# Optimization experiments

Hardware: AMD Instinct MI355X
Metric: run time of the kernel (lower is better)

Reference implementation:

```python
import jax, jax.numpy as jnp
import numpy as np

VOCAB_SIZE = 64
HIDDEN_DIM = 64
SEQ_LEN = 48
MEMORY_SLOTS = 8
DECAY_THRESHOLD = 0.05
B = 131072


def setup_inputs() -> dict:
    key = jax.random.key(0)
    ks = jax.random.split(key, 8)
    seqs = jax.random.randint(ks[0], (B, SEQ_LEN), 0, VOCAB_SIZE, dtype=jnp.int64 if jax.config.jax_enable_x64 else jnp.int32)
    query_tok = jax.random.randint(ks[1], (B,), 0, VOCAB_SIZE, dtype=seqs.dtype)
    embed = jax.random.normal(ks[2], (VOCAB_SIZE + 2, HIDDEN_DIM), dtype=jnp.float32) * 0.02
    W1 = jax.random.normal(ks[3], (HIDDEN_DIM, HIDDEN_DIM * 2), dtype=jnp.float32) * (1.0 / np.sqrt(2 * HIDDEN_DIM))
    b1 = jnp.zeros((HIDDEN_DIM,), dtype=jnp.float32)
    W2 = jax.random.normal(ks[4], (VOCAB_SIZE, HIDDEN_DIM), dtype=jnp.float32) * (1.0 / np.sqrt(HIDDEN_DIM))
    b2 = jnp.zeros((VOCAB_SIZE,), dtype=jnp.float32)
    log_stability = jnp.asarray(np.log(10.0), dtype=jnp.float32)
    return {"seqs": seqs, "query_tok": query_tok, "embed": embed,
            "W1": W1, "b1": b1, "W2": W2, "b2": b2, "log_stability": log_stability}


def reference(seqs, query_tok, embed, W1, b1, W2, b2, log_stability):
    S = jnp.exp(log_stability)
    # Final memory after the per-step decay/evict loop: last MEMORY_SLOTS tokens
    # inserted at steps t0 = SEQ_LEN-1-MEMORY_SLOTS .. SEQ_LEN-2, with final
    # ages a = [MEMORY_SLOTS-1 .. 0]. Each entry has been scaled by
    # prod_{j=0..a} exp(-j/S) = exp(-a(a+1)/(2S)); retained iff exp(-a/S) >= thr.
    ages = jnp.arange(MEMORY_SLOTS - 1, -1, -1, dtype=jnp.float32)          # [M]
    toks = seqs[:, SEQ_LEN - 1 - MEMORY_SLOTS:SEQ_LEN - 1]                  # [B, M]
    embs = embed[toks]                                                      # [B, M, D]
    keep = (jnp.exp(-ages / S) >= DECAY_THRESHOLD)                          # [M] bool
    w = jnp.exp(-ages * (ages + 1.0) / (2.0 * S)) * keep.astype(jnp.float32)
    count = jnp.maximum(jnp.sum(keep.astype(jnp.float32)), 1.0)
    mem_summary = jnp.einsum('bmd,m->bd', embs, w) / count                  # [B, D]
    q_emb = embed[query_tok]                                                # [B, D]
    h = jnp.concatenate([q_emb, mem_summary], axis=-1)                      # [B, 2D]
    h = jax.nn.relu(h @ W1.T + b1)                                          # [B, D]
    logits = h @ W2.T + b2                                                  # [B, V]
    return logits
```

## Files before the change

### kernel.cpp

```cpp
#include <hip/hip_runtime.h>

#define VOCAB 64
#define HID 64
#define SEQL 48
#define MSLOTS 8
#define BLKT 256
#define STR 68

__global__ void ebb_prep(const float* __restrict__ embed,
                         const float* __restrict__ W1,
                         const float* __restrict__ b1,
                         const float* __restrict__ log_stab,
                         float* __restrict__ ws) {
    int t = blockIdx.x;
    int tid = threadIdx.x;
    int table = tid >> 6;
    int col = tid & 63;
    const float* erow = embed + t * HID;
    const float* wrow = W1 + col * (2 * HID) + table * HID;
    float acc = (table == 0) ? b1[col] : 0.f;
#pragma unroll
    for (int k = 0; k < HID; ++k) acc = fmaf(erow[k], wrow[k], acc);
    ws[table * (VOCAB * HID) + t * HID + col] = acc;

    if (blockIdx.x == 0 && tid < MSLOTS) {
        float S = expf(log_stab[0]);
        float cnt = 0.f;
        for (int m = 0; m < MSLOTS; ++m) {
            float age = (float)(MSLOTS - 1 - m);
            cnt += (expf(-age / S) >= 0.05f) ? 1.f : 0.f;
        }
        cnt = fmaxf(cnt, 1.f);
        float age = (float)(MSLOTS - 1 - tid);
        float keep = (expf(-age / S) >= 0.05f) ? 1.f : 0.f;
        float w = expf(-age * (age + 1.f) / (2.f * S)) * keep;
        ws[2 * VOCAB * HID + tid] = w / cnt;
    }
}

__global__ __launch_bounds__(BLKT, 2)
void ebb_main(const int* __restrict__ seqs, const int* __restrict__ qtok,
              const float* __restrict__ ws, const float* __restrict__ W2,
              const float* __restrict__ b2,
              float* __restrict__ out) {
    __shared__ float sWq[VOCAB][STR];
    __shared__ float sWm[VOCAB][STR];
    __shared__ float sH[64][STR];

    int tid  = threadIdx.x;
    int lane = tid & 63;
    int wv   = tid >> 6;

    for (int i = tid; i < VOCAB * HID; i += BLKT) {
        int r = i >> 6, c = i & 63;
        sWq[r][c] = ws[i];
        sWm[r][c] = ws[VOCAB * HID + i];
    }

    float4 w2r[16];
    {
        const float4* W2v = (const float4*)(W2 + lane * HID);
#pragma unroll
        for (int j4 = 0; j4 < 16; ++j4) w2r[j4] = W2v[j4];
    }
    float bb = b2[lane];

    int row = blockIdx.x * BLKT + tid;
    const int* srow = seqs + (size_t)row * SEQL;
    int qt = qtok[row];
    int t0 = srow[39];
    int4 ta = *(const int4*)(srow + 40);
    int4 tb = *(const int4*)(srow + 44);
    int toks[MSLOTS] = {t0, ta.x, ta.y, ta.z, ta.w, tb.x, tb.y, tb.z};

    __syncthreads();

    float h[HID];
    {
        const float4* wq = (const float4*)&sWq[qt][0];
#pragma unroll
        for (int j4 = 0; j4 < 16; ++j4) {
            float4 a = wq[j4];
            h[4 * j4 + 0] = a.x; h[4 * j4 + 1] = a.y;
            h[4 * j4 + 2] = a.z; h[4 * j4 + 3] = a.w;
        }
    }
#pragma unroll
    for (int m = 0; m < MSLOTS; ++m) {
        float wwm = ws[2 * VOCAB * HID + m];
        const float4* wm = (const float4*)&sWm[toks[m]][0];
#pragma unroll
        for (int j4 = 0; j4 < 16; ++j4) {
            float4 a = wm[j4];
            h[4 * j4 + 0] = fmaf(wwm, a.x, h[4 * j4 + 0]);
            h[4 * j4 + 1] = fmaf(wwm, a.y, h[4 * j4 + 1]);
            h[4 * j4 + 2] = fmaf(wwm, a.z, h[4 * j4 + 2]);
            h[4 * j4 + 3] = fmaf(wwm, a.w, h[4 * j4 + 3]);
        }
    }
#pragma unroll
    for (int j = 0; j < HID; ++j) h[j] = fmaxf(h[j], 0.f);

    size_t obase = (size_t)blockIdx.x * BLKT * HID;
#pragma unroll 1
    for (int c = 0; c < 4; ++c) {
        if (wv == c) {
            float4* dst = (float4*)&sH[lane][0];
#pragma unroll
            for (int j4 = 0; j4 < 16; ++j4)
                dst[j4] = make_float4(h[4 * j4 + 0], h[4 * j4 + 1],
                                      h[4 * j4 + 2], h[4 * j4 + 3]);
        }
        __syncthreads();
#pragma unroll 1
        for (int r = 0; r < 16; ++r) {
            int hr = wv * 16 + r;
            const float4* hv = (const float4*)&sH[hr][0];
            float a0 = bb, a1 = 0.f, a2 = 0.f, a3 = 0.f;
#pragma unroll
            for (int j4 = 0; j4 < 16; j4 += 4) {
                float4 x0 = hv[j4 + 0], x1 = hv[j4 + 1];
                float4 x2 = hv[j4 + 2], x3 = hv[j4 + 3];
                a0 = fmaf(x0.x, w2r[j4 + 0].x, a0); a0 = fmaf(x0.y, w2r[j4 + 0].y, a0);
                a0 = fmaf(x0.z, w2r[j4 + 0].z, a0); a0 = fmaf(x0.w, w2r[j4 + 0].w, a0);
                a1 = fmaf(x1.x, w2r[j4 + 1].x, a1); a1 = fmaf(x1.y, w2r[j4 + 1].y, a1);
                a1 = fmaf(x1.z, w2r[j4 + 1].z, a1); a1 = fmaf(x1.w, w2r[j4 + 1].w, a1);
                a2 = fmaf(x2.x, w2r[j4 + 2].x, a2); a2 = fmaf(x2.y, w2r[j4 + 2].y, a2);
                a2 = fmaf(x2.z, w2r[j4 + 2].z, a2); a2 = fmaf(x2.w, w2r[j4 + 2].w, a2);
                a3 = fmaf(x3.x, w2r[j4 + 3].x, a3); a3 = fmaf(x3.y, w2r[j4 + 3].y, a3);
                a3 = fmaf(x3.z, w2r[j4 + 3].z, a3); a3 = fmaf(x3.w, w2r[j4 + 3].w, a3);
            }
            out[obase + (size_t)(c * 64 + hr) * HID + lane] = (a0 + a1) + (a2 + a3);
        }
        __syncthreads();
    }
}

extern "C" void kernel_launch(void* const* d_in, const int* in_sizes, int n_in,
                              void* d_out, int out_size, void* d_ws, size_t ws_size,
                              hipStream_t stream) {
    const int*   seqs     = (const int*)d_in[0];
    const int*   qtok     = (const int*)d_in[1];
    const float* embed    = (const float*)d_in[2];
    const float* W1       = (const float*)d_in[3];
    const float* b1       = (const float*)d_in[4];
    const float* W2       = (const float*)d_in[5];
    const float* b2       = (const float*)d_in[6];
    const float* log_stab = (const float*)d_in[7];
    float* out = (float*)d_out;
    float* ws  = (float*)d_ws;

    int B = in_sizes[1];

    ebb_prep<<<VOCAB, 2 * HID, 0, stream>>>(embed, W1, b1, log_stab, ws);

    int nblk = (B + BLKT - 1) / BLKT;
    ebb_main<<<nblk, BLKT, 0, stream>>>(seqs, qtok, ws, W2, b2, out);
}
```

Baseline: 126.8 us.

## Stage all hidden rows in reused swizzled LDS and drop per-chunk barriers

Overlays the hidden-activation staging buffer on the same shared memory as the W1 lookup tables, using a 64KB buffer and an XOR swizzle to avoid bank conflicts. All 256 rows are written at once, so the four-round write/sync/compute loop becomes a single pass where each wave handles its own 64 rows, two at a time. The W2 register load is moved after the first phase to shorten register live ranges. The 64KB LDS allocation per block may lower occupancy compared with the previous smaller footprint.

After: 118.0 us. 1.07x faster.

```diff
diff --git a/kernel.cpp b/kernel.cpp
--- a/kernel.cpp
+++ b/kernel.cpp
@@ -43,9 +43,9 @@
               const float* __restrict__ ws, const float* __restrict__ W2,
               const float* __restrict__ b2,
               float* __restrict__ out) {
-    __shared__ float sWq[VOCAB][STR];
-    __shared__ float sWm[VOCAB][STR];
-    __shared__ float sH[64][STR];
+    __shared__ __align__(16) char smem[65536];
+    float (*sWq)[STR] = (float (*)[STR])(smem);
+    float (*sWm)[STR] = (float (*)[STR])(smem + 17408);
 
     int tid  = threadIdx.x;
     int lane = tid & 63;
@@ -57,14 +57,6 @@
         sWm[r][c] = ws[VOCAB * HID + i];
     }
 
-    float4 w2r[16];
-    {
-        const float4* W2v = (const float4*)(W2 + lane * HID);
-#pragma unroll
-        for (int j4 = 0; j4 < 16; ++j4) w2r[j4] = W2v[j4];
-    }
-    float bb = b2[lane];
-
     int row = blockIdx.x * BLKT + tid;
     const int* srow = seqs + (size_t)row * SEQL;
     int qt = qtok[row];
@@ -72,6 +64,7 @@
     int4 ta = *(const int4*)(srow + 40);
     int4 tb = *(const int4*)(srow + 44);
     int toks[MSLOTS] = {t0, ta.x, ta.y, ta.z, ta.w, tb.x, tb.y, tb.z};
+    float bb = b2[lane];
 
     __syncthreads();
 
@@ -98,41 +91,68 @@
             h[4 * j4 + 3] = fmaf(wwm, a.w, h[4 * j4 + 3]);
         }
     }
+
+    __syncthreads();
+
+    {
+        unsigned rbase = (unsigned)tid * 256;
+        unsigned sw = ((unsigned)tid & 7u) << 4;
 #pragma unroll
-    for (int j = 0; j < HID; ++j) h[j] = fmaxf(h[j], 0.f);
+        for (int j4 = 0; j4 < 16; ++j4) {
+            float4 v = make_float4(fmaxf(h[4 * j4 + 0], 0.f),
+                                   fmaxf(h[4 * j4 + 1], 0.f),
+                                   fmaxf(h[4 * j4 + 2], 0.f),
+                                   fmaxf(h[4 * j4 + 3], 0.f));
+            *(float4*)(smem + (rbase + ((unsigned)(j4 * 16) ^ sw))) = v;
+        }
+    }
 
-    size_t obase = (size_t)blockIdx.x * BLKT * HID;
+    float4 w2r[16];
+    {
+        const float4* W2v = (const float4*)(W2 + lane * HID);
+#pragma unroll
+        for (int j4 = 0; j4 < 16; ++j4) w2r[j4] = W2v[j4];
+    }
+
+    size_t obase = (size_t)blockIdx.x * BLKT + (size_t)wv * 64;
 #pragma unroll 1
-    for (int c = 0; c < 4; ++c) {
-        if (wv == c) {
-            float4* dst = (float4*)&sH[lane][0];
+    for (int r = 0; r < 64; r += 2) {
+        int hr0 = wv * 64 + r, hr1 = hr0 + 1;
+        const char* p0 = smem + hr0 * 256;
+        const char* p1 = smem + hr1 * 256;
+        unsigned x0 = ((unsigned)hr0 & 7u) << 4;
+        unsigned x1 = ((unsigned)hr1 & 7u) << 4;
+        float a0 = bb, a1 = 0.f, a2 = 0.f, a3 = 0.f;
+        float c0 = bb, c1 = 0.f, c2 = 0.f, c3 = 0.f;
 #pragma unroll
-            for (int j4 = 0; j4 < 16; ++j4)
-                dst[j4] = make_float4(h[4 * j4 + 0], h[4 * j4 + 1],
-                                      h[4 * j4 + 2], h[4 * j4 + 3]);
+        for (int j4 = 0; j4 < 16; j4 += 4) {
+            float4 u0 = *(const float4*)(p0 + (((unsigned)((j4 + 0) * 16)) ^ x0));
+            float4 u1 = *(const float4*)(p0 + (((unsigned)((j4 + 1) * 16)) ^ x0));
+            float4 u2 = *(const float4*)(p0 + (((unsigned)((j4 + 2) * 16)) ^ x0));
+            float4 u3 = *(const float4*)(p0 + (((unsigned)((j4 + 3) * 16)) ^ x0));
+            float4 v0 = *(const float4*)(p1 + (((unsigned)((j4 + 0) * 16)) ^ x1));
+            float4 v1 = *(const float4*)(p1 + (((unsigned)((j4 + 1) * 16)) ^ x1));
+            float4 v2 = *(const float4*)(p1 + (((unsigned)((j4 + 2) * 16)) ^ x1));
+            float4 v3 = *(const float4*)(p1 + (((unsigned)((j4 + 3) * 16)) ^ x1));
+            a0 = fmaf(u0.x, w2r[j4 + 0].x, a0); a0 = fmaf(u0.y, w2r[j4 + 0].y, a0);
+            a0 = fmaf(u0.z, w2r[j4 + 0].z, a0); a0 = fmaf(u0.w, w2r[j4 + 0].w, a0);
+            a1 = fmaf(u1.x, w2r[j4 + 1].x, a1); a1 = fmaf(u1.y, w2r[j4 + 1].y, a1);
+            a1 = fmaf(u1.z, w2r[j4 + 1].z, a1); a1 = fmaf(u1.w, w2r[j4 + 1].w, a1);
+            a2 = fmaf(u2.x, w2r[j4 + 2].x, a2); a2 = fmaf(u2.y, w2r[j4 + 2].y, a2);
+            a2 = fmaf(u2.z, w2r[j4 + 2].z, a2); a2 = fmaf(u2.w, w2r[j4 + 2].w, a2);
+            a3 = fmaf(u3.x, w2r[j4 + 3].x, a3); a3 = fmaf(u3.y, w2r[j4 + 3].y, a3);
+            a3 = fmaf(u3.z, w2r[j4 + 3].z, a3); a3 = fmaf(u3.w, w2r[j4 + 3].w, a3);
+            c0 = fmaf(v0.x, w2r[j4 + 0].x, c0); c0 = fmaf(v0.y, w2r[j4 + 0].y, c0);
+            c0 = fmaf(v0.z, w2r[j4 + 0].z, c0); c0 = fmaf(v0.w, w2r[j4 + 0].w, c0);
+            c1 = fmaf(v1.x, w2r[j4 + 1].x, c1); c1 = fmaf(v1.y, w2r[j4 + 1].y, c1);
+            c1 = fmaf(v1.z, w2r[j4 + 1].z, c1); c1 = fmaf(v1.w, w2r[j4 + 1].w, c1);
+            c2 = fmaf(v2.x, w2r[j4 + 2].x, c2); c2 = fmaf(v2.y, w2r[j4 + 2].y, c2);
+            c2 = fmaf(v2.z, w2r[j4 + 2].z, c2); c2 = fmaf(v2.w, w2r[j4 + 2].w, c2);
+            c3 = fmaf(v3.x, w2r[j4 + 3].x, c3); c3 = fmaf(v3.y, w2r[j4 + 3].y, c3);
+            c3 = fmaf(v3.z, w2r[j4 + 3].z, c3); c3 = fmaf(v3.w, w2r[j4 + 3].w, c3);
         }
-        __syncthreads();
-#pragma unroll 1
-        for (int r = 0; r < 16; ++r) {
-            int hr = wv * 16 + r;
-            const float4* hv = (const float4*)&sH[hr][0];
-            float a0 = bb, a1 = 0.f, a2 = 0.f, a3 = 0.f;
-#pragma unroll
-            for (int j4 = 0; j4 < 16; j4 += 4) {
-                float4 x0 = hv[j4 + 0], x1 = hv[j4 + 1];
-                float4 x2 = hv[j4 + 2], x3 = hv[j4 + 3];
-                a0 = fmaf(x0.x, w2r[j4 + 0].x, a0); a0 = fmaf(x0.y, w2r[j4 + 0].y, a0);
-                a0 = fmaf(x0.z, w2r[j4 + 0].z, a0); a0 = fmaf(x0.w, w2r[j4 + 0].w, a0);
-                a1 = fmaf(x1.x, w2r[j4 + 1].x, a1); a1 = fmaf(x1.y, w2r[j4 + 1].y, a1);
-                a1 = fmaf(x1.z, w2r[j4 + 1].z, a1); a1 = fmaf(x1.w, w2r[j4 + 1].w, a1);
-                a2 = fmaf(x2.x, w2r[j4 + 2].x, a2); a2 = fmaf(x2.y, w2r[j4 + 2].y, a2);
-                a2 = fmaf(x2.z, w2r[j4 + 2].z, a2); a2 = fmaf(x2.w, w2r[j4 + 2].w, a2);
-                a3 = fmaf(x3.x, w2r[j4 + 3].x, a3); a3 = fmaf(x3.y, w2r[j4 + 3].y, a3);
-                a3 = fmaf(x3.z, w2r[j4 + 3].z, a3); a3 = fmaf(x3.w, w2r[j4 + 3].w, a3);
-            }
-            out[obase + (size_t)(c * 64 + hr) * HID + lane] = (a0 + a1) + (a2 + a3);
-        }
-        __syncthreads();
+        out[(obase + r) * HID + lane]     = (a0 + a1) + (a2 + a3);
+        out[(obase + r + 1) * HID + lane] = (c0 + c1) + (c2 + c3);
     }
 }
 
```

## Compute second GEMM with split-bf16 MFMA instead of scalar FP32 FMAs

Applied to the files above, without the earlier changes.

Replaces the per-lane scalar FP32 dot products for h·W2ᵀ with MFMA 16x16x32 bf16 instructions. Each operand is split into a high and a low bf16 part and three products are summed to approximate FP32 accuracy. All 256 hidden rows are staged at once in a swizzled 64KB shared buffer, which removes the four-chunk loop and its barriers. The cost is 64KB of LDS per block, which limits occupancy, plus conversion overhead and a small precision loss versus FP32.

Measured after the change: 102.8 us. -19.0%, faster.

```diff
diff --git a/kernel.cpp b/kernel.cpp
--- a/kernel.cpp
+++ b/kernel.cpp
@@ -6,6 +6,17 @@
 #define MSLOTS 8
 #define BLKT 256
 #define STR 68
+
+typedef __attribute__((ext_vector_type(8))) short bf16x8;
+typedef __attribute__((ext_vector_type(4))) float f32x4;
+
+__device__ __forceinline__ unsigned bf16_rne(float x) {
+    unsigned u = __float_as_uint(x);
+    return (u + 0x7FFFu + ((u >> 16) & 1u)) >> 16;
+}
+__device__ __forceinline__ float bf16f(unsigned b) {
+    return __uint_as_float(b << 16);
+}
 
 __global__ void ebb_prep(const float* __restrict__ embed,
                          const float* __restrict__ W1,
@@ -43,9 +54,9 @@
               const float* __restrict__ ws, const float* __restrict__ W2,
               const float* __restrict__ b2,
               float* __restrict__ out) {
-    __shared__ float sWq[VOCAB][STR];
-    __shared__ float sWm[VOCAB][STR];
-    __shared__ float sH[64][STR];
+    __shared__ __align__(16) char smem[65536];
+    float (*sWq)[STR] = (float (*)[STR])(smem);
+    float (*sWm)[STR] = (float (*)[STR])(smem + 17408);
 
     int tid  = threadIdx.x;
     int lane = tid & 63;
@@ -56,14 +67,6 @@
         sWq[r][c] = ws[i];
         sWm[r][c] = ws[VOCAB * HID + i];
     }
-
-    float4 w2r[16];
-    {
-        const float4* W2v = (const float4*)(W2 + lane * HID);
-#pragma unroll
-        for (int j4 = 0; j4 < 16; ++j4) w2r[j4] = W2v[j4];
-    }
-    float bb = b2[lane];
 
     int row = blockIdx.x * BLKT + tid;
     const int* srow = seqs + (size_t)row * SEQL;
@@ -98,41 +101,89 @@
             h[4 * j4 + 3] = fmaf(wwm, a.w, h[4 * j4 + 3]);
         }
     }
-#pragma unroll
-    for (int j = 0; j < HID; ++j) h[j] = fmaxf(h[j], 0.f);
-
-    size_t obase = (size_t)blockIdx.x * BLKT * HID;
+
+    __syncthreads();
+
+    {
+        unsigned rbase = (unsigned)tid * 128;
+        unsigned sw = ((unsigned)tid & 7u) << 4;
+#pragma unroll
+        for (int c8 = 0; c8 < 8; ++c8) {
+            unsigned off = ((unsigned)(c8 * 16)) ^ sw;
+            int hw[4], lw[4];
+#pragma unroll
+            for (int p = 0; p < 4; ++p) {
+                float v0 = fmaxf(h[c8 * 8 + 2 * p + 0], 0.f);
+                float v1 = fmaxf(h[c8 * 8 + 2 * p + 1], 0.f);
+                unsigned h0 = bf16_rne(v0), h1 = bf16_rne(v1);
+                unsigned l0 = bf16_rne(v0 - bf16f(h0));
+                unsigned l1 = bf16_rne(v1 - bf16f(h1));
+                hw[p] = (int)(h0 | (h1 << 16));
+                lw[p] = (int)(l0 | (l1 << 16));
+            }
+            *(int4*)(smem + (rbase + off))         = make_int4(hw[0], hw[1], hw[2], hw[3]);
+            *(int4*)(smem + 32768 + (rbase + off)) = make_int4(lw[0], lw[1], lw[2], lw[3]);
+        }
+    }
+    __builtin_amdgcn_sched_barrier(0);
+
+    bf16x8 wbh[8], wbl[8];
+    {
+        int n  = lane & 15;
+        int kg = (lane >> 4) * 8;
+#pragma unroll
+        for (int nt = 0; nt < 4; ++nt) {
+            const float* wr = W2 + (size_t)(nt * 16 + n) * HID + kg;
+#pragma unroll
+            for (int kt = 0; kt < 2; ++kt) {
+                float4 p0 = *(const float4*)(wr + kt * 32);
+                float4 p1 = *(const float4*)(wr + kt * 32 + 4);
+                float vv[8] = {p0.x, p0.y, p0.z, p0.w, p1.x, p1.y, p1.z, p1.w};
+                bf16x8 bh, bl;
+#pragma unroll
+                for (int i = 0; i < 8; ++i) {
+                    unsigned hb = bf16_rne(vv[i]);
+                    bh[i] = (short)hb;
+                    bl[i] = (short)bf16_rne(vv[i] - bf16f(hb));
+                }
+                wbh[nt * 2 + kt] = bh;
+                wbl[nt * 2 + kt] = bl;
+            }
+        }
+    }
+    float bcol[4];
+#pragma unroll
+    for (int nt = 0; nt < 4; ++nt) bcol[nt] = b2[nt * 16 + (lane & 15)];
+
 #pragma unroll 1
-    for (int c = 0; c < 4; ++c) {
-        if (wv == c) {
-            float4* dst = (float4*)&sH[lane][0];
-#pragma unroll
-            for (int j4 = 0; j4 < 16; ++j4)
-                dst[j4] = make_float4(h[4 * j4 + 0], h[4 * j4 + 1],
-                                      h[4 * j4 + 2], h[4 * j4 + 3]);
-        }
-        __syncthreads();
-#pragma unroll 1
-        for (int r = 0; r < 16; ++r) {
-            int hr = wv * 16 + r;
-            const float4* hv = (const float4*)&sH[hr][0];
-            float a0 = bb, a1 = 0.f, a2 = 0.f, a3 = 0.f;
-#pragma unroll
-            for (int j4 = 0; j4 < 16; j4 += 4) {
-                float4 x0 = hv[j4 + 0], x1 = hv[j4 + 1];
-                float4 x2 = hv[j4 + 2], x3 = hv[j4 + 3];
-                a0 = fmaf(x0.x, w2r[j4 + 0].x, a0); a0 = fmaf(x0.y, w2r[j4 + 0].y, a0);
-                a0 = fmaf(x0.z, w2r[j4 + 0].z, a0); a0 = fmaf(x0.w, w2r[j4 + 0].w, a0);
-                a1 = fmaf(x1.x, w2r[j4 + 1].x, a1); a1 = fmaf(x1.y, w2r[j4 + 1].y, a1);
-                a1 = fmaf(x1.z, w2r[j4 + 1].z, a1); a1 = fmaf(x1.w, w2r[j4 + 1].w, a1);
-                a2 = fmaf(x2.x, w2r[j4 + 2].x, a2); a2 = fmaf(x2.y, w2r[j4 + 2].y, a2);
-                a2 = fmaf(x2.z, w2r[j4 + 2].z, a2); a2 = fmaf(x2.w, w2r[j4 + 2].w, a2);
-                a3 = fmaf(x3.x, w2r[j4 + 3].x, a3); a3 = fmaf(x3.y, w2r[j4 + 3].y, a3);
-                a3 = fmaf(x3.z, w2r[j4 + 3].z, a3); a3 = fmaf(x3.w, w2r[j4 + 3].w, a3);
+    for (int mt = 0; mt < 4; ++mt) {
+        int r0 = wv * 64 + mt * 16;
+        unsigned arow  = (unsigned)(r0 + (lane & 15));
+        unsigned abase = arow * 128;
+        unsigned asw   = (arow & 7u) << 4;
+        bf16x8 ah[2], al[2];
+#pragma unroll
+        for (int kt = 0; kt < 2; ++kt) {
+            unsigned off = ((unsigned)(((lane >> 4) + 4 * kt) * 16)) ^ asw;
+            ah[kt] = *(const bf16x8*)(smem + (abase + off));
+            al[kt] = *(const bf16x8*)(smem + 32768 + (abase + off));
+        }
+#pragma unroll
+        for (int nt = 0; nt < 4; ++nt) {
+            f32x4 acc = {bcol[nt], bcol[nt], bcol[nt], bcol[nt]};
+#pragma unroll
+            for (int kt = 0; kt < 2; ++kt) {
+                acc = __builtin_amdgcn_mfma_f32_16x16x32_bf16(ah[kt], wbh[nt * 2 + kt], acc, 0, 0, 0);
+                acc = __builtin_amdgcn_mfma_f32_16x16x32_bf16(ah[kt], wbl[nt * 2 + kt], acc, 0, 0, 0);
+                acc = __builtin_amdgcn_mfma_f32_16x16x32_bf16(al[kt], wbh[nt * 2 + kt], acc, 0, 0, 0);
             }
-            out[obase + (size_t)(c * 64 + hr) * HID + lane] = (a0 + a1) + (a2 + a3);
-        }
-        __syncthreads();
+            size_t ob = ((size_t)blockIdx.x * BLKT + (size_t)(r0 + (lane >> 4) * 4)) * HID
+                        + (size_t)(nt * 16 + (lane & 15));
+            out[ob + 0 * HID] = acc[0];
+            out[ob + 1 * HID] = acc[1];
+            out[ob + 2 * HID] = acc[2];
+            out[ob + 3 * HID] = acc[3];
+        }
     }
 }
 
```
